# Kernel tuning notes

Measured on AMD Instinct MI355X. Metric: run time of the kernel, lower is better.

## Reference

```python
import jax, jax.numpy as jnp
import numpy as np

B, T, H, A = 64, 512, 1024, 256  # T == max_sen_len by construction of attention_u
PAD_VAL = -2.0 ** 22


def setup_inputs() -> dict:
    key = jax.random.key(0)
    k1, k2, k3, k4 = jax.random.split(key, 4)
    inputs = jax.random.normal(k1, (B, T, H), dtype=jnp.float32)
    sen_len = jax.random.randint(k2, (B,), 1, T + 1, dtype=jnp.int32)
    W = jax.random.normal(k3, (H, A), dtype=jnp.float32) * (1.0 / np.sqrt(H))
    b = jnp.zeros((A,), dtype=jnp.float32)
    U = jax.random.normal(k4, (A, T), dtype=jnp.float32) * (1.0 / np.sqrt(A))
    return {"inputs": inputs, "sen_len": sen_len, "W": W, "b": b, "U": U}


def reference(inputs, sen_len, W, b, U):
    # Dense with tanh: [B,T,H] @ [H,A] -> [B,T,A]
    alpha = jnp.tanh(jnp.einsum('bth,ha->bta', inputs, W) + b)
    # Score against attention_u: [B,T,A] @ [A,T] -> [B,T,T]
    scores = jnp.einsum('bta,as->bts', alpha, U)
    # sequence mask over last (key) dim, broadcast over query dim
    mask = jnp.arange(T)[None, :] < sen_len[:, None]        # [B,T]
    scores = jnp.where(mask[:, None, :], scores, jnp.float32(PAD_VAL))
    p = jax.nn.softmax(scores, axis=-1)                     # [B,T,T]
    # Weighted sum pooling: [B,T,T] @ [B,T,H] -> [B,T,H]
    Z = jnp.einsum('bts,bsh->bth', p, inputs)
    # dropout: is_training=False -> identity
    return Z
```

## Files before the change

### kernel.cpp

```cpp
#include <hip/hip_runtime.h>
#include <hip/hip_bf16.h>

typedef short short8 __attribute__((ext_vector_type(8)));
typedef short short4v __attribute__((ext_vector_type(4)));
typedef float f32x4 __attribute__((ext_vector_type(4)));
typedef __bf16 bf16x8 __attribute__((ext_vector_type(8)));

template <int ROWS>
__device__ __forceinline__ void stage2(const __hip_bfloat16* __restrict__ g,
                                       int ld, short* lds, int t) {
    const int w = t >> 6;
    const int lane = t & 63;
#pragma unroll
    for (int i = 0; i < ROWS / 64; ++i) {
        const int cb = i * 512 + w * 64;
        const int c = cb + lane;
        const int row = c >> 3;
        const int kc = (c & 7) ^ (row & 7);
        __builtin_amdgcn_global_load_lds((const void*)(g + (long)row * ld + kc * 8),
                                         (void*)(lds + cb * 8), 16, 0, 0);
    }
}

__global__ __launch_bounds__(512, 4) void gemm_xw_kernel(
    const float* __restrict__ Xf,
    const __hip_bfloat16* __restrict__ Wt,
    __hip_bfloat16* __restrict__ alpha,
    const float* __restrict__ bias) {
    __shared__ __align__(16) short smB[3][8192];
    __shared__ __align__(16) short smA[2][8192];

    int bx = blockIdx.x, by = blockIdx.y;
    {
        const int nx = gridDim.x, ny = gridDim.y;
        const int nwg = nx * ny;
        const int lin = bx + nx * by;
        const int swz = (lin & 7) * (nwg >> 3) + (lin >> 3);
        bx = swz % nx;
        by = swz / nx;
    }

    const int t = threadIdx.x;
    const int w = t >> 6, lane = t & 63;
    const int wm = w >> 1, wn = w & 1;
    const int fr = lane & 15, quad = lane >> 4;

    const float* Ab = Xf + (long)by * 128 * 1024;
    const __hip_bfloat16* Bb = Wt + (long)bx * 128 * 1024;

    int acs[2], arow[2], akc[2];
#pragma unroll
    for (int i = 0; i < 2; ++i) {
        acs[i] = i * 512 + t;
        arow[i] = acs[i] >> 3;
        akc[i] = ((acs[i] & 7) ^ (arow[i] & 7)) * 8;
    }

    f32x4 acc[2][4] = {};
    float4 rAs[2][2][2];

#define XW_ISSUE_B(KT, BUF) stage2<128>(Bb + (KT) * 64, 1024, &smB[BUF][0], t);

#define XW_LOAD_A(KT, S)                                                        \
    _Pragma("unroll") for (int i = 0; i < 2; ++i) {                             \
        const float* src = Ab + (long)arow[i] * 1024 + (KT) * 64 + akc[i];      \
        rAs[S][i][0] = *(const float4*)(src);                                   \
        rAs[S][i][1] = *(const float4*)(src + 4);                               \
    }

#define XW_WRITE_A(BUF, S)                                                      \
    _Pragma("unroll") for (int i = 0; i < 2; ++i) {                             \
        __hip_bfloat16 tmp[8] __attribute__((aligned(16)));                     \
        tmp[0] = __float2bfloat16(rAs[S][i][0].x);                              \
        tmp[1] = __float2bfloat16(rAs[S][i][0].y);                              \
        tmp[2] = __float2bfloat16(rAs[S][i][0].z);                              \
        tmp[3] = __float2bfloat16(rAs[S][i][0].w);                              \
        tmp[4] = __float2bfloat16(rAs[S][i][1].x);                              \
        tmp[5] = __float2bfloat16(rAs[S][i][1].y);                              \
        tmp[6] = __float2bfloat16(rAs[S][i][1].z);                              \
        tmp[7] = __float2bfloat16(rAs[S][i][1].w);                              \
        *(short8*)(void*)&smA[BUF][acs[i] * 8] = *(short8*)(void*)tmp;          \
    }

    XW_LOAD_A(0, 0)
    XW_ISSUE_B(0, 0)
    XW_ISSUE_B(1, 1)
    XW_WRITE_A(0, 0)
    XW_LOAD_A(1, 1)
    XW_LOAD_A(2, 0)
    __builtin_amdgcn_sched_barrier(0);
    asm volatile("s_waitcnt vmcnt(10)" ::: "memory");
    asm volatile("s_waitcnt lgkmcnt(0)" ::: "memory");
    __builtin_amdgcn_s_barrier();
    __builtin_amdgcn_sched_barrier(0);

#define XW_STEP(K)                                                              \
    {                                                                           \
        if ((K) + 2 < 16) { XW_ISSUE_B((K) + 2, ((K) + 2) % 3) }                \
        const short* At_ = &smA[(K) % 2][0];                                    \
        const short* Bt_ = &smB[(K) % 3][0];                                    \
        _Pragma("unroll") for (int ks = 0; ks < 2; ++ks) {                      \
            bf16x8 af[2], bfv[4];                                               \
            const int kc = ks * 4 + quad;                                       \
            _Pragma("unroll") for (int m = 0; m < 2; ++m) {                     \
                const int row = wm * 32 + m * 16 + fr;                          \
                const int chunk = row * 8 + (kc ^ (row & 7));                   \
                af[m] = *(const bf16x8*)(const void*)(At_ + chunk * 8);         \
            }                                                                   \
            _Pragma("unroll") for (int n = 0; n < 4; ++n) {                     \
                const int row = wn * 64 + n * 16 + fr;                          \
                const int chunk = row * 8 + (kc ^ (row & 7));                   \
                bfv[n] = *(const bf16x8*)(const void*)(Bt_ + chunk * 8);        \
            }                                                                   \
            _Pragma("unroll") for (int m = 0; m < 2; ++m)                       \
                _Pragma("unroll") for (int n = 0; n < 4; ++n)                   \
                    acc[m][n] = __builtin_amdgcn_mfma_f32_16x16x32_bf16(        \
                        af[m], bfv[n], acc[m][n], 0, 0, 0);                     \
        }                                                                       \
        if ((K) + 1 < 16) { XW_WRITE_A(((K) + 1) % 2, ((K) + 1) & 1) }          \
        if ((K) + 3 < 16) { XW_LOAD_A((K) + 3, ((K) + 1) & 1) }                 \
        __builtin_amdgcn_sched_barrier(0);                                      \
        if ((K) + 3 < 16) {                                                     \
            asm volatile("s_waitcnt vmcnt(10)" ::: "memory");                   \
        } else if ((K) + 2 < 16) {                                              \
            asm volatile("s_waitcnt vmcnt(6)" ::: "memory");                    \
        } else if ((K) + 1 < 16) {                                              \
            asm volatile("s_waitcnt vmcnt(0)" ::: "memory");                    \
        }                                                                       \
        if ((K) + 1 < 16) {                                                     \
            asm volatile("s_waitcnt lgkmcnt(0)" ::: "memory");                  \
            __builtin_amdgcn_s_barrier();                                       \
            __builtin_amdgcn_sched_barrier(0);                                  \
        }                                                                       \
    }

    XW_STEP(0)  XW_STEP(1)  XW_STEP(2)  XW_STEP(3)
    XW_STEP(4)  XW_STEP(5)  XW_STEP(6)  XW_STEP(7)
    XW_STEP(8)  XW_STEP(9)  XW_STEP(10) XW_STEP(11)
    XW_STEP(12) XW_STEP(13) XW_STEP(14) XW_STEP(15)
#undef XW_STEP
#undef XW_ISSUE_B
#undef XW_LOAD_A
#undef XW_WRITE_A

    const long rowBase = (long)by * 128 + wm * 32;
    const int colBase = bx * 128 + wn * 64;
#pragma unroll
    for (int m = 0; m < 2; ++m) {
#pragma unroll
        for (int n = 0; n < 4; ++n) {
            const int col = colBase + n * 16 + fr;
            const float bv = bias[col];
#pragma unroll
            for (int j = 0; j < 4; ++j) {
                const long row = rowBase + m * 16 + quad * 4 + j;
                alpha[row * 256 + col] = __float2bfloat16(tanhf(acc[m][n][j] + bv));
            }
        }
    }
}

__global__ __launch_bounds__(512, 2) void gemm_pv_kernel(
    const __hip_bfloat16* __restrict__ P,
    const float* __restrict__ Xf,
    float* __restrict__ Z) {
    __shared__ __align__(16) short smA[3][8192];
    __shared__ __align__(16) float smB[3][4096];

    int bx = blockIdx.x, by = blockIdx.y, bz = blockIdx.z;
    {
        const int nx = gridDim.x, ny = gridDim.y;
        const int nwg = nx * ny * gridDim.z;
        const int lin = bx + nx * (by + ny * bz);
        const int swz = (lin & 7) * (nwg >> 3) + (lin >> 3);
        bx = swz % nx;
        const int r = swz / nx;
        by = r % ny;
        bz = r / ny;
    }

    const int t = threadIdx.x;
    const int w = t >> 6, lane = t & 63;
    const int wm = w >> 1, wn = w & 1;
    const int fr = lane & 15, quad = lane >> 4;

    const __hip_bfloat16* Ab = P + ((long)bz * 512 + by * 256) * 512;
    const float* Bb = Xf + (long)bz * 512 * 1024 + bx * 128;

    int acb[2], arow[2], akc[2];
#pragma unroll
    for (int i = 0; i < 2; ++i) {
        acb[i] = i * 512 + w * 64;
        const int s = acb[i] + lane;
        arow[i] = s >> 2;
        akc[i] = ((s & 3) ^ ((arow[i] >> 1) & 3)) * 8;
    }

    f32x4 acc[4][4] = {};

#define PV_ISSUE_A(KT, BUF)                                                     \
    _Pragma("unroll") for (int i = 0; i < 2; ++i)                               \
        __builtin_amdgcn_global_load_lds(                                       \
            (const void*)(Ab + (long)arow[i] * 512 + (KT) * 32 + akc[i]),       \
            (void*)(&smA[BUF][acb[i] * 8]), 16, 0, 0);

#define PV_ISSUE_B(KT, BUF)                                                     \
    _Pragma("unroll") for (int i = 0; i < 2; ++i) {                             \
        const int g = i * 512 + t;                                              \
        __builtin_amdgcn_global_load_lds(                                       \
            (const void*)(Bb + (long)((KT) * 32 + (g >> 5)) * 1024 + (g & 31) * 4), \
            (void*)(&smB[BUF][(i * 512 + w * 64) * 4]), 16, 0, 0);              \
    }

    PV_ISSUE_A(0, 0)
    PV_ISSUE_B(0, 0)
    PV_ISSUE_A(1, 1)
    PV_ISSUE_B(1, 1)
    __builtin_amdgcn_sched_barrier(0);
    asm volatile("s_waitcnt vmcnt(4)" ::: "memory");
    __builtin_amdgcn_s_barrier();
    __builtin_amdgcn_sched_barrier(0);

#define PV_STEP(K)                                                              \
    {                                                                           \
        if ((K) + 2 < 16) {                                                     \
            PV_ISSUE_A((K) + 2, ((K) + 2) % 3)                                  \
            PV_ISSUE_B((K) + 2, ((K) + 2) % 3)                                  \
        }                                                                       \
        const short* At_ = &smA[(K) % 3][0];                                    \
        const float* Bt_ = &smB[(K) % 3][0];                                    \
        bf16x8 bfv[4];                                                          \
        _Pragma("unroll") for (int n = 0; n < 4; ++n) {                         \
            const float* col = Bt_ + quad * 8 * 128 + wn * 64 + n * 16 + fr;    \
            __hip_bfloat16 tmp[8] __attribute__((aligned(16)));                 \
            _Pragma("unroll") for (int j = 0; j < 8; ++j)                       \
                tmp[j] = __float2bfloat16(col[j * 128]);                        \
            bfv[n] = *(bf16x8*)(void*)tmp;                                      \
        }                                                                       \
        _Pragma("unroll") for (int m = 0; m < 4; ++m) {                         \
            const int row = wm * 64 + m * 16 + fr;                              \
            const int slot = row * 4 + (quad ^ ((row >> 1) & 3));               \
            const bf16x8 af = *(const bf16x8*)(const void*)(At_ + slot * 8);    \
            _Pragma("unroll") for (int n = 0; n < 4; ++n)                       \
                acc[m][n] = __builtin_amdgcn_mfma_f32_16x16x32_bf16(            \
                    af, bfv[n], acc[m][n], 0, 0, 0);                            \
        }                                                                       \
        __builtin_amdgcn_sched_barrier(0);                                      \
        if ((K) + 2 < 16) {                                                     \
            asm volatile("s_waitcnt vmcnt(4)" ::: "memory");                    \
        } else if ((K) + 1 < 16) {                                              \
            asm volatile("s_waitcnt vmcnt(0)" ::: "memory");                    \
        }                                                                       \
        if ((K) + 1 < 16) {                                                     \
            __builtin_amdgcn_s_barrier();                                       \
            __builtin_amdgcn_sched_barrier(0);                                  \
        }                                                                       \
    }

    PV_STEP(0)  PV_STEP(1)  PV_STEP(2)  PV_STEP(3)
    PV_STEP(4)  PV_STEP(5)  PV_STEP(6)  PV_STEP(7)
    PV_STEP(8)  PV_STEP(9)  PV_STEP(10) PV_STEP(11)
    PV_STEP(12) PV_STEP(13) PV_STEP(14) PV_STEP(15)
#undef PV_STEP
#undef PV_ISSUE_A
#undef PV_ISSUE_B

    const long rowBase = (long)bz * 512 + by * 256 + wm * 64;
    const int colBase = bx * 128 + wn * 64;
#pragma unroll
    for (int m = 0; m < 4; ++m) {
#pragma unroll
        for (int n = 0; n < 4; ++n) {
            const int col = colBase + n * 16 + fr;
#pragma unroll
            for (int j = 0; j < 4; ++j) {
                const long row = rowBase + m * 16 + quad * 4 + j;
                Z[row * 1024 + col] = acc[m][n][j];
            }
        }
    }
}

__global__ __launch_bounds__(256) void transpose_cvt_kernel(const float* __restrict__ in,
                                                            __hip_bfloat16* __restrict__ out,
                                                            int R, int C) {
    const int o = blockIdx.x * 256 + threadIdx.x;
    if (o >= R * C) return;
    const int c = o / R;
    const int r = o - c * R;
    out[o] = __float2bfloat16(in[(long)r * C + c]);
}

__global__ __launch_bounds__(512, 4) void score_softmax_kernel(
    const __hip_bfloat16* __restrict__ Aa,
    const __hip_bfloat16* __restrict__ Ut,
    __hip_bfloat16* __restrict__ P,
    const int* __restrict__ sen) {
    __shared__ __align__(16) short At[2048 * 8];
    __shared__ float red[2][64][9];

    const int t = threadIdx.x;
    const int w = t >> 6, lane = t & 63;
    const int fr = lane & 15, quad = lane >> 4;
    const long row0 = (long)blockIdx.x * 64;
    const __hip_bfloat16* Ab = Aa + row0 * 256;

#pragma unroll
    for (int i = 0; i < 4; ++i) {
        const int cb = i * 512 + w * 64;
        const int c = cb + lane;
        const int row = c >> 5;
        const int kc = (c & 31) ^ (row & 7);
        __builtin_amdgcn_global_load_lds(
            (const void*)(Ab + (long)row * 256 + kc * 8),
            (void*)(At + cb * 8), 16, 0, 0);
    }

    f32x4 acc[4][4] = {};
    bf16x8 bfvs[2][4];

#define SM_LOAD_B(KT, S)                                                        \
    _Pragma("unroll") for (int n = 0; n < 4; ++n)                               \
        bfvs[S][n] = *(const bf16x8*)(const void*)(                             \
            Ut + (w * 64 + n * 16 + fr) * 256 + (KT) * 32 + quad * 8);

    SM_LOAD_B(0, 0)
    SM_LOAD_B(1, 1)
    __builtin_amdgcn_sched_barrier(0);
    asm volatile("s_waitcnt vmcnt(8)" ::: "memory");
    __builtin_amdgcn_s_barrier();
    __builtin_amdgcn_sched_barrier(0);

#define SM_STEP(KT)                                                             \
    {                                                                           \
        bf16x8 af[4];                                                           \
        _Pragma("unroll") for (int m = 0; m < 4; ++m) {                         \
            const int row = m * 16 + fr;                                        \
            const int g = row * 32 + (((KT) * 4 + quad) ^ (row & 7));           \
            af[m] = *(const bf16x8*)(const void*)(At + g * 8);                  \
        }                                                                       \
        _Pragma("unroll") for (int m = 0; m < 4; ++m)                           \
            _Pragma("unroll") for (int n = 0; n < 4; ++n)                       \
                acc[m][n] = __builtin_amdgcn_mfma_f32_16x16x32_bf16(            \
                    af[m], bfvs[(KT) & 1][n], acc[m][n], 0, 0, 0);              \
        if ((KT) + 2 < 8) { SM_LOAD_B((KT) + 2, (KT) & 1) }                     \
    }

    SM_STEP(0) SM_STEP(1) SM_STEP(2) SM_STEP(3)
    SM_STEP(4) SM_STEP(5) SM_STEP(6) SM_STEP(7)
#undef SM_STEP
#undef SM_LOAD_B
    __syncthreads();

    const int L = sen[row0 >> 9];
    bool valid[4];
#pragma unroll
    for (int n = 0; n < 4; ++n) valid[n] = (w * 64 + n * 16 + fr) < L;

    float mx[4][4];
#pragma unroll
    for (int m = 0; m < 4; ++m)
#pragma unroll
        for (int j = 0; j < 4; ++j) {
            float v = -3.0e38f;
#pragma unroll
            for (int n = 0; n < 4; ++n)
                if (valid[n]) v = fmaxf(v, acc[m][n][j]);
#pragma unroll
            for (int off = 8; off >= 1; off >>= 1) v = fmaxf(v, __shfl_xor(v, off, 64));
            mx[m][j] = v;
        }
    if (fr == 0) {
#pragma unroll
        for (int m = 0; m < 4; ++m)
#pragma unroll
            for (int j = 0; j < 4; ++j) red[0][m * 16 + quad * 4 + j][w] = mx[m][j];
    }
    __syncthreads();
    float rmax[4][4];
#pragma unroll
    for (int m = 0; m < 4; ++m)
#pragma unroll
        for (int j = 0; j < 4; ++j) {
            const int row = m * 16 + quad * 4 + j;
            float v = red[0][row][0];
#pragma unroll
            for (int ww = 1; ww < 8; ++ww) v = fmaxf(v, red[0][row][ww]);
            rmax[m][j] = v;
        }

    float sum[4][4];
#pragma unroll
    for (int m = 0; m < 4; ++m)
#pragma unroll
        for (int j = 0; j < 4; ++j) {
            float s = 0.f;
#pragma unroll
            for (int n = 0; n < 4; ++n) {
                float e = valid[n] ? __expf(acc[m][n][j] - rmax[m][j]) : 0.f;
                acc[m][n][j] = e;
                s += e;
            }
#pragma unroll
            for (int off = 8; off >= 1; off >>= 1) s += __shfl_xor(s, off, 64);
            sum[m][j] = s;
        }
    if (fr == 0) {
#pragma unroll
        for (int m = 0; m < 4; ++m)
#pragma unroll
            for (int j = 0; j < 4; ++j) red[1][m * 16 + quad * 4 + j][w] = sum[m][j];
    }
    __syncthreads();
#pragma unroll
    for (int m = 0; m < 4; ++m)
#pragma unroll
        for (int j = 0; j < 4; ++j) {
            const int row = m * 16 + quad * 4 + j;
            float s = 0.f;
#pragma unroll
            for (int ww = 0; ww < 8; ++ww) s += red[1][row][ww];
            const float inv = 1.f / s;
#pragma unroll
            for (int n = 0; n < 4; ++n)
                P[(row0 + row) * 512 + w * 64 + n * 16 + fr] =
                    __float2bfloat16(acc[m][n][j] * inv);
        }
}

extern "C" void kernel_launch(void* const* d_in, const int* in_sizes, int n_in,
                              void* d_out, int out_size, void* d_ws, size_t ws_size,
                              hipStream_t stream) {
    const float* X = (const float*)d_in[0];
    const int* sen = (const int*)d_in[1];
    const float* W = (const float*)d_in[2];
    const float* bias = (const float*)d_in[3];
    const float* U = (const float*)d_in[4];
    float* out = (float*)d_out;

    const int B = 64, T = 512, H = 1024, A = 256;
    const long M = (long)B * T;

    char* ws = (char*)d_ws;
    __hip_bfloat16* Pbf = (__hip_bfloat16*)ws;
    __hip_bfloat16* Wt = (__hip_bfloat16*)(ws + M * T * 2);
    __hip_bfloat16* Ut = (__hip_bfloat16*)((char*)Wt + (long)H * A * 2);

    __hip_bfloat16* alpha = (__hip_bfloat16*)((char*)d_out + M * H * 2);

    transpose_cvt_kernel<<<(H * A) / 256, 256, 0, stream>>>(W, Wt, H, A);
    transpose_cvt_kernel<<<(A * T) / 256, 256, 0, stream>>>(U, Ut, A, T);
    gemm_xw_kernel<<<dim3(2, 256), 512, 0, stream>>>(X, Wt, alpha, bias);
    score_softmax_kernel<<<(int)(M / 64), 512, 0, stream>>>(alpha, Ut, Pbf, sen);
    gemm_pv_kernel<<<dim3(H / 128, T / 256, B), 512, 0, stream>>>(Pbf, X, out);
}
```

Baseline: 148.2 us.

## Emit transposed bf16 X from XW GEMM and feed it to PV GEMM

The first GEMM already converts X tiles to bf16 in shared memory. Blocks with bx==0 now also write a transposed bf16 copy of X to workspace. The PV GEMM then reads this bf16 transposed X instead of fp32 X, which removes the per-step fp32-to-bf16 conversion and strided LDS gathers and halves B-operand traffic. PV is also retiled to 128x128 with a simpler double-buffered loop and higher occupancy. The cost is an extra 64 MB bf16 write in the first kernel and added LDS reads for half its blocks, which may unbalance that kernel.

```diff
diff --git a/kernel.cpp b/kernel.cpp
--- a/kernel.cpp
+++ b/kernel.cpp
@@ -26,7 +26,8 @@
     const float* __restrict__ Xf,
     const __hip_bfloat16* __restrict__ Wt,
     __hip_bfloat16* __restrict__ alpha,
-    const float* __restrict__ bias) {
+    const float* __restrict__ bias,
+    __hip_bfloat16* __restrict__ XtOut) {
     __shared__ __align__(16) short smB[3][8192];
     __shared__ __align__(16) short smA[2][8192];
 
@@ -39,6 +40,8 @@
         bx = swz % nx;
         by = swz / nx;
     }
+    const int byg = by;
+    const bool doxt = (bx == 0);
 
     const int t = threadIdx.x;
     const int w = t >> 6, lane = t & 63;
@@ -80,6 +83,25 @@
         tmp[6] = __float2bfloat16(rAs[S][i][1].z);                              \
         tmp[7] = __float2bfloat16(rAs[S][i][1].w);                              \
         *(short8*)(void*)&smA[BUF][acs[i] * 8] = *(short8*)(void*)tmp;          \
+    }
+
+#define XW_XT(K)                                                                \
+    if (doxt) {                                                                 \
+        const short* Att = &smA[(K) % 2][0];                                    \
+        const int hl = t & 63;                                                  \
+        _Pragma("unroll") for (int p = 0; p < 2; ++p) {                         \
+            const int trun = (t >> 6) * 2 + p;                                  \
+            __hip_bfloat16 tmp2[8] __attribute__((aligned(16)));                \
+            _Pragma("unroll") for (int j = 0; j < 8; ++j) {                     \
+                const int row = trun * 8 + j;                                   \
+                const int u = (hl >> 3) ^ (row & 7);                            \
+                tmp2[j] = ((const __hip_bfloat16*)(const void*)Att)             \
+                              [row * 64 + u * 8 + (hl & 7)];                    \
+            }                                                                   \
+            *(short8*)(void*)(XtOut +                                           \
+                (((long)byg * 1024) + (K) * 64 + hl) * 128 + trun * 8) =        \
+                *(short8*)(void*)tmp2;                                          \
+        }                                                                       \
     }
 
     XW_LOAD_A(0, 0)
@@ -117,15 +139,19 @@
                     acc[m][n] = __builtin_amdgcn_mfma_f32_16x16x32_bf16(        \
                         af[m], bfv[n], acc[m][n], 0, 0, 0);                     \
         }                                                                       \
+        XW_XT(K)                                                                \
         if ((K) + 1 < 16) { XW_WRITE_A(((K) + 1) % 2, ((K) + 1) & 1) }          \
         if ((K) + 3 < 16) { XW_LOAD_A((K) + 3, ((K) + 1) & 1) }                 \
         __builtin_amdgcn_sched_barrier(0);                                      \
         if ((K) + 3 < 16) {                                                     \
-            asm volatile("s_waitcnt vmcnt(10)" ::: "memory");                   \
+            if (doxt) asm volatile("s_waitcnt vmcnt(12)" ::: "memory");         \
+            else      asm volatile("s_waitcnt vmcnt(10)" ::: "memory");         \
         } else if ((K) + 2 < 16) {                                              \
-            asm volatile("s_waitcnt vmcnt(6)" ::: "memory");                    \
+            if (doxt) asm volatile("s_waitcnt vmcnt(8)" ::: "memory");          \
+            else      asm volatile("s_waitcnt vmcnt(6)" ::: "memory");          \
         } else if ((K) + 1 < 16) {                                              \
-            asm volatile("s_waitcnt vmcnt(0)" ::: "memory");                    \
+            if (doxt) asm volatile("s_waitcnt vmcnt(2)" ::: "memory");          \
+            else      asm volatile("s_waitcnt vmcnt(0)" ::: "memory");          \
         }                                                                       \
         if ((K) + 1 < 16) {                                                     \
             asm volatile("s_waitcnt lgkmcnt(0)" ::: "memory");                  \
@@ -139,6 +165,7 @@
     XW_STEP(8)  XW_STEP(9)  XW_STEP(10) XW_STEP(11)
     XW_STEP(12) XW_STEP(13) XW_STEP(14) XW_STEP(15)
 #undef XW_STEP
+#undef XW_XT
 #undef XW_ISSUE_B
 #undef XW_LOAD_A
 #undef XW_WRITE_A
@@ -160,12 +187,12 @@
     }
 }
 
-__global__ __launch_bounds__(512, 2) void gemm_pv_kernel(
+__global__ __launch_bounds__(512, 4) void gemm_pv_kernel(
     const __hip_bfloat16* __restrict__ P,
-    const float* __restrict__ Xf,
+    const __hip_bfloat16* __restrict__ Xt,
     float* __restrict__ Z) {
-    __shared__ __align__(16) short smA[3][8192];
-    __shared__ __align__(16) float smB[3][4096];
+    __shared__ __align__(16) short smA[2][4096];
+    __shared__ __align__(16) short smB[2][4096];
 
     int bx = blockIdx.x, by = blockIdx.y, bz = blockIdx.z;
     {
@@ -184,91 +211,59 @@
     const int wm = w >> 1, wn = w & 1;
     const int fr = lane & 15, quad = lane >> 4;
 
-    const __hip_bfloat16* Ab = P + ((long)bz * 512 + by * 256) * 512;
-    const float* Bb = Xf + (long)bz * 512 * 1024 + bx * 128;
-
-    int acb[2], arow[2], akc[2];
-#pragma unroll
-    for (int i = 0; i < 2; ++i) {
-        acb[i] = i * 512 + w * 64;
-        const int s = acb[i] + lane;
-        arow[i] = s >> 2;
-        akc[i] = ((s & 3) ^ ((arow[i] >> 1) & 3)) * 8;
-    }
-
-    f32x4 acc[4][4] = {};
-
-#define PV_ISSUE_A(KT, BUF)                                                     \
-    _Pragma("unroll") for (int i = 0; i < 2; ++i)                               \
+    const __hip_bfloat16* Ab = P + ((long)bz * 512 + by * 128) * 512;
+
+    const int grow = t >> 2;
+    const int gkc = ((t & 3) ^ ((grow >> 1) & 3)) * 8;
+
+#define PV_STAGE(KT, BUF)                                                       \
+    {                                                                           \
         __builtin_amdgcn_global_load_lds(                                       \
-            (const void*)(Ab + (long)arow[i] * 512 + (KT) * 32 + akc[i]),       \
-            (void*)(&smA[BUF][acb[i] * 8]), 16, 0, 0);
-
-#define PV_ISSUE_B(KT, BUF)                                                     \
-    _Pragma("unroll") for (int i = 0; i < 2; ++i) {                             \
-        const int g = i * 512 + t;                                              \
-        __builtin_amdgcn_global_load_lds(                                       \
-            (const void*)(Bb + (long)((KT) * 32 + (g >> 5)) * 1024 + (g & 31) * 4), \
-            (void*)(&smB[BUF][(i * 512 + w * 64) * 4]), 16, 0, 0);              \
-    }
-
-    PV_ISSUE_A(0, 0)
-    PV_ISSUE_B(0, 0)
-    PV_ISSUE_A(1, 1)
-    PV_ISSUE_B(1, 1)
-    __builtin_amdgcn_sched_barrier(0);
-    asm volatile("s_waitcnt vmcnt(4)" ::: "memory");
-    __builtin_amdgcn_s_barrier();
-    __builtin_amdgcn_sched_barrier(0);
-
-#define PV_STEP(K)                                                              \
-    {                                                                           \
-        if ((K) + 2 < 16) {                                                     \
-            PV_ISSUE_A((K) + 2, ((K) + 2) % 3)                                  \
-            PV_ISSUE_B((K) + 2, ((K) + 2) % 3)                                  \
-        }                                                                       \
-        const short* At_ = &smA[(K) % 3][0];                                    \
-        const float* Bt_ = &smB[(K) % 3][0];                                    \
-        bf16x8 bfv[4];                                                          \
-        _Pragma("unroll") for (int n = 0; n < 4; ++n) {                         \
-            const float* col = Bt_ + quad * 8 * 128 + wn * 64 + n * 16 + fr;    \
-            __hip_bfloat16 tmp[8] __attribute__((aligned(16)));                 \
-            _Pragma("unroll") for (int j = 0; j < 8; ++j)                       \
-                tmp[j] = __float2bfloat16(col[j * 128]);                        \
-            bfv[n] = *(bf16x8*)(void*)tmp;                                      \
-        }                                                                       \
-        _Pragma("unroll") for (int m = 0; m < 4; ++m) {                         \
-            const int row = wm * 64 + m * 16 + fr;                              \
-            const int slot = row * 4 + (quad ^ ((row >> 1) & 3));               \
-            const bf16x8 af = *(const bf16x8*)(const void*)(At_ + slot * 8);    \
-            _Pragma("unroll") for (int n = 0; n < 4; ++n)                       \
-                acc[m][n] = __builtin_amdgcn_mfma_f32_16x16x32_bf16(            \
-                    af, bfv[n], acc[m][n], 0, 0, 0);                            \
-        }                                                                       \
-        __builtin_amdgcn_sched_barrier(0);                                      \
-        if ((K) + 2 < 16) {                                                     \
-            asm volatile("s_waitcnt vmcnt(4)" ::: "memory");                    \
-        } else if ((K) + 1 < 16) {                                              \
-            asm volatile("s_waitcnt vmcnt(0)" ::: "memory");                    \
-        }                                                                       \
-        if ((K) + 1 < 16) {                                                     \
-            __builtin_amdgcn_s_barrier();                                       \
-            __builtin_amdgcn_sched_barrier(0);                                  \
-        }                                                                       \
-    }
-
-    PV_STEP(0)  PV_STEP(1)  PV_STEP(2)  PV_STEP(3)
-    PV_STEP(4)  PV_STEP(5)  PV_STEP(6)  PV_STEP(7)
-    PV_STEP(8)  PV_STEP(9)  PV_STEP(10) PV_STEP(11)
-    PV_STEP(12) PV_STEP(13) PV_STEP(14) PV_STEP(15)
-#undef PV_STEP
-#undef PV_ISSUE_A
-#undef PV_ISSUE_B
-
-    const long rowBase = (long)bz * 512 + by * 256 + wm * 64;
+            (const void*)(Ab + (long)grow * 512 + (KT) * 32 + gkc),             \
+            (void*)(&smA[BUF][t * 8]), 16, 0, 0);                               \
+        const __hip_bfloat16* bsrc = Xt +                                       \
+            ((long)(bz * 4 + ((KT) >> 2)) * 1024 + bx * 128 + grow) * 128 +     \
+            ((KT) & 3) * 32 + gkc;                                              \
+        __builtin_amdgcn_global_load_lds((const void*)bsrc,                     \
+                                         (void*)(&smB[BUF][t * 8]), 16, 0, 0);  \
+    }
+
+    f32x4 acc[2][4] = {};
+
+    PV_STAGE(0, 0)
+    __syncthreads();
+
+    int cur = 0;
+    for (int kt = 0; kt < 16; ++kt) {
+        if (kt + 1 < 16) PV_STAGE(kt + 1, cur ^ 1)
+        const short* At_ = &smA[cur][0];
+        const short* Bt_ = &smB[cur][0];
+        bf16x8 bfv[4];
+#pragma unroll
+        for (int n = 0; n < 4; ++n) {
+            const int row = wn * 64 + n * 16 + fr;
+            const int slot = row * 4 + (quad ^ ((row >> 1) & 3));
+            bfv[n] = *(const bf16x8*)(const void*)(Bt_ + slot * 8);
+        }
+#pragma unroll
+        for (int m = 0; m < 2; ++m) {
+            const int row = wm * 32 + m * 16 + fr;
+            const int slot = row * 4 + (quad ^ ((row >> 1) & 3));
+            const bf16x8 af = *(const bf16x8*)(const void*)(At_ + slot * 8);
+#pragma unroll
+            for (int n = 0; n < 4; ++n)
+                acc[m][n] = __builtin_amdgcn_mfma_f32_16x16x32_bf16(
+                    af, bfv[n], acc[m][n], 0, 0, 0);
+        }
+        __syncthreads();
+        cur ^= 1;
+    }
+#undef PV_STAGE
+
+    const long rowBase = (long)bz * 512 + by * 128 + wm * 32;
     const int colBase = bx * 128 + wn * 64;
 #pragma unroll
-    for (int m = 0; m < 4; ++m) {
+    for (int m = 0; m < 2; ++m) {
 #pragma unroll
         for (int n = 0; n < 4; ++n) {
             const int col = colBase + n * 16 + fr;
@@ -443,14 +438,15 @@
 
     char* ws = (char*)d_ws;
     __hip_bfloat16* Pbf = (__hip_bfloat16*)ws;
-    __hip_bfloat16* Wt = (__hip_bfloat16*)(ws + M * T * 2);
+    __hip_bfloat16* Xtb = (__hip_bfloat16*)(ws + M * T * 2);
+    __hip_bfloat16* Wt = (__hip_bfloat16*)(ws + M * T * 2 + M * H * 2);
     __hip_bfloat16* Ut = (__hip_bfloat16*)((char*)Wt + (long)H * A * 2);
 
     __hip_bfloat16* alpha = (__hip_bfloat16*)((char*)d_out + M * H * 2);
 
     transpose_cvt_kernel<<<(H * A) / 256, 256, 0, stream>>>(W, Wt, H, A);
     transpose_cvt_kernel<<<(A * T) / 256, 256, 0, stream>>>(U, Ut, A, T);
-    gemm_xw_kernel<<<dim3(2, 256), 512, 0, stream>>>(X, Wt, alpha, bias);
+    gemm_xw_kernel<<<dim3(2, 256), 512, 0, stream>>>(X, Wt, alpha, bias, Xtb);
     score_softmax_kernel<<<(int)(M / 64), 512, 0, stream>>>(alpha, Ut, Pbf, sen);
-    gemm_pv_kernel<<<dim3(H / 128, T / 256, B), 512, 0, stream>>>(Pbf, X, out);
-}
+    gemm_pv_kernel<<<dim3(8, 4, B), 512, 0, stream>>>(Pbf, Xtb, out);
+}
```

Result: slower. 170.9 us (+15.3%).

## Shorten XW A-prefetch depth and swizzle PV B tile in LDS

Applied to the files above, without the earlier changes.

In the X·W GEMM, the fp32 A prefetch drops from two register stages to one, so A is loaded two tiles ahead instead of three and the vmcnt waits are retuned. This cuts register pressure and may help occupancy, at the cost of less latency hiding for A loads. In the P·V kernel, the fp32 B tile is written to LDS with an XOR swizzle on 4-float chunks keyed by row group, and reads apply the matching swizzle. This is meant to reduce LDS bank conflicts in the strided column reads.

```diff
diff --git a/kernel.cpp b/kernel.cpp
--- a/kernel.cpp
+++ b/kernel.cpp
@@ -57,88 +57,86 @@
     }
 
     f32x4 acc[2][4] = {};
-    float4 rAs[2][2][2];
+    float4 rA[2][2];
 
 #define XW_ISSUE_B(KT, BUF) stage2<128>(Bb + (KT) * 64, 1024, &smB[BUF][0], t);
 
-#define XW_LOAD_A(KT, S)                                                        \
+#define XW_LOAD_A(KT)                                                           \
     _Pragma("unroll") for (int i = 0; i < 2; ++i) {                             \
         const float* src = Ab + (long)arow[i] * 1024 + (KT) * 64 + akc[i];      \
-        rAs[S][i][0] = *(const float4*)(src);                                   \
-        rAs[S][i][1] = *(const float4*)(src + 4);                               \
-    }
-
-#define XW_WRITE_A(BUF, S)                                                      \
+        rA[i][0] = *(const float4*)(src);                                       \
+        rA[i][1] = *(const float4*)(src + 4);                                   \
+    }
+
+#define XW_WRITE_A(BUF)                                                         \
     _Pragma("unroll") for (int i = 0; i < 2; ++i) {                             \
         __hip_bfloat16 tmp[8] __attribute__((aligned(16)));                     \
-        tmp[0] = __float2bfloat16(rAs[S][i][0].x);                              \
-        tmp[1] = __float2bfloat16(rAs[S][i][0].y);                              \
-        tmp[2] = __float2bfloat16(rAs[S][i][0].z);                              \
-        tmp[3] = __float2bfloat16(rAs[S][i][0].w);                              \
-        tmp[4] = __float2bfloat16(rAs[S][i][1].x);                              \
-        tmp[5] = __float2bfloat16(rAs[S][i][1].y);                              \
-        tmp[6] = __float2bfloat16(rAs[S][i][1].z);                              \
-        tmp[7] = __float2bfloat16(rAs[S][i][1].w);                              \
+        tmp[0] = __float2bfloat16(rA[i][0].x);                                  \
+        tmp[1] = __float2bfloat16(rA[i][0].y);                                  \
+        tmp[2] = __float2bfloat16(rA[i][0].z);                                  \
+        tmp[3] = __float2bfloat16(rA[i][0].w);                                  \
+        tmp[4] = __float2bfloat16(rA[i][1].x);                                  \
+        tmp[5] = __float2bfloat16(rA[i][1].y);                                  \
+        tmp[6] = __float2bfloat16(rA[i][1].z);                                  \
+        tmp[7] = __float2bfloat16(rA[i][1].w);                                  \
         *(short8*)(void*)&smA[BUF][acs[i] * 8] = *(short8*)(void*)tmp;          \
     }
 
-    XW_LOAD_A(0, 0)
     XW_ISSUE_B(0, 0)
     XW_ISSUE_B(1, 1)
-    XW_WRITE_A(0, 0)
-    XW_LOAD_A(1, 1)
-    XW_LOAD_A(2, 0)
-    __builtin_amdgcn_sched_barrier(0);
-    asm volatile("s_waitcnt vmcnt(10)" ::: "memory");
+    XW_LOAD_A(0)
+    XW_WRITE_A(0)
+    XW_LOAD_A(1)
+    __builtin_amdgcn_sched_barrier(0);
+    asm volatile("s_waitcnt vmcnt(4)" ::: "memory");
     asm volatile("s_waitcnt lgkmcnt(0)" ::: "memory");
     __builtin_amdgcn_s_barrier();
     __builtin_amdgcn_sched_barrier(0);
 
-#define XW_STEP(K)                                                              \
-    {                                                                           \
-        if ((K) + 2 < 16) { XW_ISSUE_B((K) + 2, ((K) + 2) % 3) }                \
-        const short* At_ = &smA[(K) % 2][0];                                    \
-        const short* Bt_ = &smB[(K) % 3][0];                                    \
-        _Pragma("unroll") for (int ks = 0; ks < 2; ++ks) {                      \
-            bf16x8 af[2], bfv[4];                                               \
-            const int kc = ks * 4 + quad;                                       \
-            _Pragma("unroll") for (int m = 0; m < 2; ++m) {                     \
-                const int row = wm * 32 + m * 16 + fr;                          \
-                const int chunk = row * 8 + (kc ^ (row & 7));                   \
-                af[m] = *(const bf16x8*)(const void*)(At_ + chunk * 8);         \
-            }                                                                   \
-            _Pragma("unroll") for (int n = 0; n < 4; ++n) {                     \
-                const int row = wn * 64 + n * 16 + fr;                          \
-                const int chunk = row * 8 + (kc ^ (row & 7));                   \
-                bfv[n] = *(const bf16x8*)(const void*)(Bt_ + chunk * 8);        \
-            }                                                                   \
-            _Pragma("unroll") for (int m = 0; m < 2; ++m)                       \
-                _Pragma("unroll") for (int n = 0; n < 4; ++n)                   \
-                    acc[m][n] = __builtin_amdgcn_mfma_f32_16x16x32_bf16(        \
-                        af[m], bfv[n], acc[m][n], 0, 0, 0);                     \
-        }                                                                       \
-        if ((K) + 1 < 16) { XW_WRITE_A(((K) + 1) % 2, ((K) + 1) & 1) }          \
-        if ((K) + 3 < 16) { XW_LOAD_A((K) + 3, ((K) + 1) & 1) }                 \
-        __builtin_amdgcn_sched_barrier(0);                                      \
-        if ((K) + 3 < 16) {                                                     \
-            asm volatile("s_waitcnt vmcnt(10)" ::: "memory");                   \
-        } else if ((K) + 2 < 16) {                                              \
-            asm volatile("s_waitcnt vmcnt(6)" ::: "memory");                    \
-        } else if ((K) + 1 < 16) {                                              \
-            asm volatile("s_waitcnt vmcnt(0)" ::: "memory");                    \
-        }                                                                       \
-        if ((K) + 1 < 16) {                                                     \
-            asm volatile("s_waitcnt lgkmcnt(0)" ::: "memory");                  \
-            __builtin_amdgcn_s_barrier();                                       \
-            __builtin_amdgcn_sched_barrier(0);                                  \
-        }                                                                       \
-    }
-
-    XW_STEP(0)  XW_STEP(1)  XW_STEP(2)  XW_STEP(3)
-    XW_STEP(4)  XW_STEP(5)  XW_STEP(6)  XW_STEP(7)
-    XW_STEP(8)  XW_STEP(9)  XW_STEP(10) XW_STEP(11)
-    XW_STEP(12) XW_STEP(13) XW_STEP(14) XW_STEP(15)
-#undef XW_STEP
+#pragma unroll
+    for (int k = 0; k < 16; ++k) {
+        if (k + 2 < 16) XW_ISSUE_B(k + 2, (k + 2) % 3)
+        {
+            const short* At = &smA[k % 2][0];
+            const short* Bt = &smB[k % 3][0];
+#pragma unroll
+            for (int ks = 0; ks < 2; ++ks) {
+                bf16x8 af[2], bfv[4];
+                const int kc = ks * 4 + quad;
+#pragma unroll
+                for (int m = 0; m < 2; ++m) {
+                    const int row = wm * 32 + m * 16 + fr;
+                    const int chunk = row * 8 + (kc ^ (row & 7));
+                    af[m] = *(const bf16x8*)(const void*)(At + chunk * 8);
+                }
+#pragma unroll
+                for (int n = 0; n < 4; ++n) {
+                    const int row = wn * 64 + n * 16 + fr;
+                    const int chunk = row * 8 + (kc ^ (row & 7));
+                    bfv[n] = *(const bf16x8*)(const void*)(Bt + chunk * 8);
+                }
+#pragma unroll
+                for (int m = 0; m < 2; ++m)
+#pragma unroll
+                    for (int n = 0; n < 4; ++n)
+                        acc[m][n] = __builtin_amdgcn_mfma_f32_16x16x32_bf16(
+                            af[m], bfv[n], acc[m][n], 0, 0, 0);
+            }
+        }
+        if (k + 1 < 16) XW_WRITE_A((k + 1) % 2)
+        if (k + 2 < 16) XW_LOAD_A(k + 2)
+        __builtin_amdgcn_sched_barrier(0);
+        if (k + 2 < 16) {
+            asm volatile("s_waitcnt vmcnt(6)" ::: "memory");
+        } else if (k + 1 < 16) {
+            asm volatile("s_waitcnt vmcnt(0)" ::: "memory");
+        }
+        if (k + 1 < 16) {
+            asm volatile("s_waitcnt lgkmcnt(0)" ::: "memory");
+            __builtin_amdgcn_s_barrier();
+            __builtin_amdgcn_sched_barrier(0);
+        }
+    }
 #undef XW_ISSUE_B
 #undef XW_LOAD_A
 #undef XW_WRITE_A
@@ -207,8 +205,10 @@
 #define PV_ISSUE_B(KT, BUF)                                                     \
     _Pragma("unroll") for (int i = 0; i < 2; ++i) {                             \
         const int g = i * 512 + t;                                              \
+        const int s_ = g >> 5;                                                  \
+        const int csrc = (g & 31) ^ ((s_ >> 3) << 1);                           \
         __builtin_amdgcn_global_load_lds(                                       \
-            (const void*)(Bb + (long)((KT) * 32 + (g >> 5)) * 1024 + (g & 31) * 4), \
+            (const void*)(Bb + (long)((KT) * 32 + s_) * 1024 + csrc * 4),       \
             (void*)(&smB[BUF][(i * 512 + w * 64) * 4]), 16, 0, 0);              \
     }
 
@@ -231,10 +231,12 @@
         const float* Bt_ = &smB[(K) % 3][0];                                    \
         bf16x8 bfv[4];                                                          \
         _Pragma("unroll") for (int n = 0; n < 4; ++n) {                         \
-            const float* col = Bt_ + quad * 8 * 128 + wn * 64 + n * 16 + fr;    \
+            const int h = wn * 64 + n * 16 + fr;                                \
+            const float* colp = Bt_ + quad * 8 * 128 +                          \
+                                (((h >> 2) ^ (quad << 1)) << 2) + (h & 3);      \
             __hip_bfloat16 tmp[8] __attribute__((aligned(16)));                 \
             _Pragma("unroll") for (int j = 0; j < 8; ++j)                       \
-                tmp[j] = __float2bfloat16(col[j * 128]);                        \
+                tmp[j] = __float2bfloat16(colp[j * 128]);                       \
             bfv[n] = *(bf16x8*)(void*)tmp;                                      \
         }                                                                       \
         _Pragma("unroll") for (int m = 0; m < 4; ++m) {                         \
```

New measurement: 148.8 us. Within noise of the previous version (+0.4%).
